# Optimization experiments

Measured on AMD Instinct MI355X. Metric: run time of the kernel, lower is better.

## Reference

```python
import jax, jax.numpy as jnp
import numpy as np

G = 16        # num_groups = num_features // num_channels
CG = 16       # channels per group (num_channels)
EPS = 1e-3


def setup_inputs() -> dict:
    key = jax.random.key(0)
    k1, = jax.random.split(key, 1)
    N, C, H, W = 64, 256, 56, 56
    X = jax.random.normal(k1, (N, C, H, W), dtype=jnp.float32)
    weight = jnp.ones((1, C, 1, 1), dtype=jnp.float32)
    bias = jnp.zeros((1, C, 1, 1), dtype=jnp.float32)
    return {"X": X, "weight": weight, "bias": bias}


def reference(X, weight, bias):
    N, C, H, W = X.shape
    # [N,C,H,W] -> [C, N*H*W] -> groups [G, CG, m]
    x = jnp.transpose(X, (1, 0, 2, 3)).reshape(G, CG, -1)
    m = x.shape[-1]
    mean = jnp.mean(x, axis=-1, keepdims=True)            # [G, CG, 1]
    xc = x - mean                                          # [G, CG, m]
    # sigma = eps*I + (1/m) * xc @ xc^T   (per group)
    sigma = EPS * jnp.eye(CG, dtype=X.dtype) + jnp.einsum('gcm,gdm->gcd', xc, xc) / m
    u, eig, _ = jnp.linalg.svd(sigma)                      # symmetric PSD -> SVD == eig-decomp
    # wm = u @ diag(eig^-1/2) @ u^T
    wm = jnp.einsum('gcd,gd,ged->gce', u, jax.lax.rsqrt(eig), u)  # [G, CG, CG]
    xn = jnp.einsum('gce,gem->gcm', wm, xc)                # whitened
    Xn = xn.reshape(C, N, H, W).transpose(1, 0, 2, 3)      # back to [N,C,H,W]
    return Xn * weight + bias
```

## Files before the change

### kernel.cpp

```cpp
#include <hip/hip_runtime.h>

#define NG   16
#define CG   16
#define NB   64
#define CC   256
#define HW   3136
#define HW4  784
#define MTOT (NB*HW)
#define Q4   (NB*HW4)
#define EPSV 1e-3f
#define NTRI 136
#define NRED (CG+NTRI)

#define WS_CROSS 256
#define WS_WMW   2432
#define WS_OB    6528

__global__ __launch_bounds__(256, 1) void stats_kernel(const float* __restrict__ X,
                                                       float* __restrict__ ws) {
    const int g   = blockIdx.y;
    const int tid = threadIdx.x;
    const float4* X4 = (const float4*)X;

    float cross[NTRI];
    float csum[CG];
#pragma unroll
    for (int i = 0; i < NTRI; ++i) cross[i] = 0.f;
#pragma unroll
    for (int c = 0; c < CG; ++c) csum[c] = 0.f;

#pragma unroll 1
    for (int it = 0; it < 7; ++it) {
        int q4 = it * 7168 + blockIdx.x * 256 + tid;
        int n  = q4 / HW4;
        int p4 = q4 - n * HW4;
        int base = n * (CC * HW4) + (g * CG) * HW4 + p4;

        float4 v[CG];
#pragma unroll
        for (int c = 0; c < CG; ++c) v[c] = X4[base + c * HW4];

#pragma unroll
        for (int c = 0; c < CG; ++c)
            csum[c] += (v[c].x + v[c].y) + (v[c].z + v[c].w);

        int i = 0;
#pragma unroll
        for (int c = 0; c < CG; ++c) {
#pragma unroll
            for (int d = c; d < CG; ++d) {
                cross[i] += v[c].x * v[d].x + v[c].y * v[d].y +
                            v[c].z * v[d].z + v[c].w * v[d].w;
                ++i;
            }
        }
    }

    const int lane = tid & 63;
    const int w    = tid >> 6;
#pragma unroll
    for (int c = 0; c < CG; ++c) {
        float v = csum[c];
        v += __shfl_xor(v, 32); v += __shfl_xor(v, 16); v += __shfl_xor(v, 8);
        v += __shfl_xor(v, 4);  v += __shfl_xor(v, 2);  v += __shfl_xor(v, 1);
        csum[c] = v;
    }
#pragma unroll
    for (int i = 0; i < NTRI; ++i) {
        float v = cross[i];
        v += __shfl_xor(v, 32); v += __shfl_xor(v, 16); v += __shfl_xor(v, 8);
        v += __shfl_xor(v, 4);  v += __shfl_xor(v, 2);  v += __shfl_xor(v, 1);
        cross[i] = v;
    }

    __shared__ float part[4][NRED];
    if (lane == 0) {
#pragma unroll
        for (int c = 0; c < CG; ++c) part[w][c] = csum[c];
#pragma unroll
        for (int i = 0; i < NTRI; ++i) part[w][CG + i] = cross[i];
    }
    __syncthreads();
    if (tid < NRED) {
        float s = part[0][tid] + part[1][tid] + part[2][tid] + part[3][tid];
        if (tid < CG) atomicAdd(&ws[g * CG + tid], s);
        else          atomicAdd(&ws[WS_CROSS + g * NTRI + (tid - CG)], s);
    }
}

__global__ __launch_bounds__(256) void newton_kernel(const float* __restrict__ weight,
                                                     const float* __restrict__ bias,
                                                     float* __restrict__ ws) {
    __shared__ float Y[CG][CG + 1], Z[CG][CG + 1], T[CG][CG + 1];
    __shared__ float mean_s[CG];
    __shared__ float red[256];
    __shared__ float s_norm;

    const int g   = blockIdx.x;
    const int tid = threadIdx.x;
    const int c   = tid >> 4;
    const int d   = tid & 15;

    if (tid < CG) mean_s[tid] = ws[g * CG + tid] * (1.0f / MTOT);
    __syncthreads();

    const int cc = min(c, d), dd = max(c, d);
    const int idx = cc * CG + dd - (cc * (cc + 1)) / 2;
    float sig = ws[WS_CROSS + g * NTRI + idx] * (1.0f / MTOT)
              - mean_s[c] * mean_s[d] + ((c == d) ? EPSV : 0.f);

    red[tid] = sig * sig;
    __syncthreads();
    for (int s = 128; s > 0; s >>= 1) {
        if (tid < s) red[tid] += red[tid + s];
        __syncthreads();
    }
    if (tid == 0) s_norm = sqrtf(red[0]);
    __syncthreads();
    const float s = s_norm;

    Y[c][d] = sig / s;
    Z[c][d] = (c == d) ? 1.f : 0.f;
    __syncthreads();

    for (int itn = 0; itn < 12; ++itn) {
        float t = 0.f;
#pragma unroll
        for (int k = 0; k < CG; ++k) t += Z[c][k] * Y[k][d];
        t = ((c == d) ? 3.f : 0.f) - t;
        __syncthreads();
        T[c][d] = t;
        __syncthreads();
        float yn = 0.f, zn = 0.f;
#pragma unroll
        for (int k = 0; k < CG; ++k) {
            yn += Y[c][k] * T[k][d];
            zn += T[c][k] * Z[k][d];
        }
        __syncthreads();
        Y[c][d] = 0.5f * yn;
        Z[c][d] = 0.5f * zn;
        __syncthreads();
    }

    const float wm  = Z[c][d] / sqrtf(s);
    const float w   = weight[g * CG + c];
    const float wmw = wm * w;
    ws[WS_WMW + g * 256 + c * CG + d] = wmw;

    T[c][d] = wmw * mean_s[d];
    __syncthreads();
    if (d == 0) {
        float acc = 0.f;
#pragma unroll
        for (int k = 0; k < CG; ++k) acc += T[c][k];
        ws[WS_OB + g * CG + c] = bias[g * CG + c] - acc;
    }
}

__global__ __launch_bounds__(256, 4) void apply_kernel(const float* __restrict__ X,
                                                       const float* __restrict__ ws,
                                                       float* __restrict__ out) {
    __shared__ float wmw_s[CG][CG];
    __shared__ float ob_s[CG];

    const int g   = blockIdx.y;
    const int tid = threadIdx.x;

    wmw_s[tid >> 4][tid & 15] = ws[WS_WMW + g * 256 + tid];
    if (tid < CG) ob_s[tid] = ws[WS_OB + g * CG + tid];
    __syncthreads();

    const int q4 = blockIdx.x * 256 + tid;
    const int n  = q4 / HW4;
    const int p4 = q4 - n * HW4;
    const int base = n * (CC * HW4) + (g * CG) * HW4 + p4;

    const float4* X4 = (const float4*)X;
    float4* O4 = (float4*)out;

    float4 v[CG];
#pragma unroll
    for (int cdx = 0; cdx < CG; ++cdx) v[cdx] = X4[base + cdx * HW4];

#pragma unroll
    for (int c = 0; c < CG; ++c) {
        const float o = ob_s[c];
        float4 acc;
        acc.x = o; acc.y = o; acc.z = o; acc.w = o;
#pragma unroll
        for (int d = 0; d < CG; ++d) {
            const float w = wmw_s[c][d];
            acc.x += w * v[d].x; acc.y += w * v[d].y;
            acc.z += w * v[d].z; acc.w += w * v[d].w;
        }
        O4[base + c * HW4] = acc;
    }
}

extern "C" void kernel_launch(void* const* d_in, const int* in_sizes, int n_in,
                              void* d_out, int out_size, void* d_ws, size_t ws_size,
                              hipStream_t stream) {
    const float* X      = (const float*)d_in[0];
    const float* weight = (const float*)d_in[1];
    const float* bias   = (const float*)d_in[2];
    float* out = (float*)d_out;
    float* ws  = (float*)d_ws;

    hipMemsetAsync(ws, 0, WS_WMW * sizeof(float), stream);

    dim3 g1(28, NG);
    stats_kernel<<<g1, 256, 0, stream>>>(X, ws);

    newton_kernel<<<NG, 256, 0, stream>>>(weight, bias, ws);

    dim3 g3(196, NG);
    apply_kernel<<<g3, 256, 0, stream>>>(X, ws, out);
}
```

Before: 420.5 us.

## Double-buffer stats loads with fewer blocks and nontemporal apply stores

The stats kernel drops from 28 to 16 blocks per group and processes twelve strided chunks with a software-pipelined double buffer, plus a tail chunk handled by four blocks. This is meant to overlap global loads with the FMA-heavy cross-product accumulation. The apply kernel issues its input loads before the shared-memory weight setup and barrier, and writes output with nontemporal stores to avoid cache pollution. The cost is higher register pressure from the two buffers and fewer resident waves in the stats kernel.

```diff
diff --git a/kernel.cpp b/kernel.cpp
--- a/kernel.cpp
+++ b/kernel.cpp
@@ -12,15 +12,23 @@
 #define NTRI 136
 #define NRED (CG+NTRI)
 
+typedef float vfloat4 __attribute__((ext_vector_type(4)));
+
 #define WS_CROSS 256
 #define WS_WMW   2432
 #define WS_OB    6528
+
+#define SBLK 16
+#define TPG  (SBLK*256)
+#define FULL_IT 12
 
 __global__ __launch_bounds__(256, 1) void stats_kernel(const float* __restrict__ X,
                                                        float* __restrict__ ws) {
     const int g   = blockIdx.y;
     const int tid = threadIdx.x;
-    const float4* X4 = (const float4*)X;
+    const float4* __restrict__ X4 = (const float4*)X;
+    const int q0  = blockIdx.x * 256 + tid;
+    const int gq  = g * CG * HW4;
 
     float cross[NTRI];
     float csum[CG];
@@ -29,32 +37,51 @@
 #pragma unroll
     for (int c = 0; c < CG; ++c) csum[c] = 0.f;
 
+    float4 va[CG], vb[CG];
+
+#define LOADV(V, QQ)                                                       \
+    {                                                                      \
+        const int q4_ = (QQ);                                              \
+        const int n_  = q4_ / HW4;                                         \
+        const int p4_ = q4_ - n_ * HW4;                                    \
+        const float4* __restrict__ pp_ = X4 + n_ * (CC * HW4) + gq + p4_;  \
+        _Pragma("unroll")                                                  \
+        for (int c_ = 0; c_ < CG; ++c_) V[c_] = pp_[c_ * HW4];             \
+    }
+
+#define ACCV(V)                                                            \
+    {                                                                      \
+        _Pragma("unroll")                                                  \
+        for (int c_ = 0; c_ < CG; ++c_)                                    \
+            csum[c_] += (V[c_].x + V[c_].y) + (V[c_].z + V[c_].w);         \
+        int i_ = 0;                                                        \
+        _Pragma("unroll")                                                  \
+        for (int c_ = 0; c_ < CG; ++c_) {                                  \
+            _Pragma("unroll")                                              \
+            for (int d_ = c_; d_ < CG; ++d_, ++i_)                         \
+                cross[i_] += V[c_].x * V[d_].x + V[c_].y * V[d_].y +       \
+                             V[c_].z * V[d_].z + V[c_].w * V[d_].w;        \
+        }                                                                  \
+    }
+
+    const bool tail = (blockIdx.x < 4);
+
+    LOADV(va, q0);
 #pragma unroll 1
-    for (int it = 0; it < 7; ++it) {
-        int q4 = it * 7168 + blockIdx.x * 256 + tid;
-        int n  = q4 / HW4;
-        int p4 = q4 - n * HW4;
-        int base = n * (CC * HW4) + (g * CG) * HW4 + p4;
-
-        float4 v[CG];
-#pragma unroll
-        for (int c = 0; c < CG; ++c) v[c] = X4[base + c * HW4];
-
-#pragma unroll
-        for (int c = 0; c < CG; ++c)
-            csum[c] += (v[c].x + v[c].y) + (v[c].z + v[c].w);
-
-        int i = 0;
-#pragma unroll
-        for (int c = 0; c < CG; ++c) {
-#pragma unroll
-            for (int d = c; d < CG; ++d) {
-                cross[i] += v[c].x * v[d].x + v[c].y * v[d].y +
-                            v[c].z * v[d].z + v[c].w * v[d].w;
-                ++i;
-            }
-        }
-    }
+    for (int p = 0; p < FULL_IT / 2 - 1; ++p) {
+        LOADV(vb, q0 + (2 * p + 1) * TPG);
+        ACCV(va);
+        LOADV(va, q0 + (2 * p + 2) * TPG);
+        ACCV(vb);
+    }
+    LOADV(vb, q0 + 11 * TPG);
+    ACCV(va);
+    if (tail) LOADV(va, q0 + FULL_IT * TPG);
+    ACCV(vb);
+    if (tail) ACCV(va);
+
+#undef LOADV
+#undef ACCV
 
     const int lane = tid & 63;
     const int w    = tid >> 6;
@@ -167,26 +194,26 @@
     const int g   = blockIdx.y;
     const int tid = threadIdx.x;
 
-    wmw_s[tid >> 4][tid & 15] = ws[WS_WMW + g * 256 + tid];
-    if (tid < CG) ob_s[tid] = ws[WS_OB + g * CG + tid];
-    __syncthreads();
-
     const int q4 = blockIdx.x * 256 + tid;
     const int n  = q4 / HW4;
     const int p4 = q4 - n * HW4;
     const int base = n * (CC * HW4) + (g * CG) * HW4 + p4;
 
-    const float4* X4 = (const float4*)X;
-    float4* O4 = (float4*)out;
+    const float4* __restrict__ X4 = (const float4*)X;
+    vfloat4* __restrict__ O4 = (vfloat4*)out;
 
     float4 v[CG];
 #pragma unroll
     for (int cdx = 0; cdx < CG; ++cdx) v[cdx] = X4[base + cdx * HW4];
+
+    wmw_s[tid >> 4][tid & 15] = ws[WS_WMW + g * 256 + tid];
+    if (tid < CG) ob_s[tid] = ws[WS_OB + g * CG + tid];
+    __syncthreads();
 
 #pragma unroll
     for (int c = 0; c < CG; ++c) {
         const float o = ob_s[c];
-        float4 acc;
+        vfloat4 acc;
         acc.x = o; acc.y = o; acc.z = o; acc.w = o;
 #pragma unroll
         for (int d = 0; d < CG; ++d) {
@@ -194,7 +221,7 @@
             acc.x += w * v[d].x; acc.y += w * v[d].y;
             acc.z += w * v[d].z; acc.w += w * v[d].w;
         }
-        O4[base + c * HW4] = acc;
+        __builtin_nontemporal_store(acc, &O4[base + c * HW4]);
     }
 }
 
@@ -207,13 +234,13 @@
     float* out = (float*)d_out;
     float* ws  = (float*)d_ws;
 
-    hipMemsetAsync(ws, 0, WS_WMW * sizeof(float), stream);
-
-    dim3 g1(28, NG);
+    (void)hipMemsetAsync(ws, 0, WS_WMW * sizeof(float), stream);
+
+    dim3 g1(SBLK, NG);
     stats_kernel<<<g1, 256, 0, stream>>>(X, ws);
 
     newton_kernel<<<NG, 256, 0, stream>>>(weight, bias, ws);
 
     dim3 g3(196, NG);
-    apply_kernel<<<g3, 256, 0, stream>>>(X, ws, out);
-}
+    apply_kernel<<<g3, 196 == 196 ? 256 : 256, 0, stream>>>(X, ws, out);
+}
```

Result: faster. 400.0 us (-4.9%).
